# Kernel optimization log

Hardware: AMD Instinct MI355X
Metric: run time of the kernel (lower is better)

The kernel has to match this reference:

```python
import jax, jax.numpy as jnp
import numpy as np

B, S, H = 8, 128, 768  # batch, seq_len, hidden (guide==vis)
EPS = 1e-12


def setup_inputs() -> dict:
    key = jax.random.key(0)
    ks = jax.random.split(key, 5)
    return {
        "seq_hiddens_x": jax.random.normal(ks[0], (B, S, H), jnp.float32),
        "seq_hiddens_y": jax.random.normal(ks[1], (B, S, H), jnp.float32),
        "cat_W": jax.random.normal(ks[2], (H, 2 * H), jnp.float32) * 0.02,
        "cat_b": jnp.zeros((H,), jnp.float32),
        "beta": jnp.zeros((H,), jnp.float32),
        "gamma": jnp.ones((H,), jnp.float32),
        "beta_W": jax.random.normal(ks[3], (H, H), jnp.float32) * 0.02,
        "gamma_W": jax.random.normal(ks[4], (H, H), jnp.float32) * 0.02,
    }


def reference(seq_hiddens_x, seq_hiddens_y, cat_W, cat_b, beta, gamma, beta_W, gamma_W):
    s = seq_hiddens_x.shape[1]
    # upper_reg2seq: flatten upper-triangular (i<=j) pairs, row-major
    ii, jj = np.triu_indices(s)
    guide = seq_hiddens_x[:, ii, :]    # (B, P, H)
    visible = seq_hiddens_y[:, jj, :]  # (B, P, H)

    # 'cat' branch: relu(Linear([guide; visible]))
    cat_pre = jax.nn.relu(
        jnp.einsum('bph,oh->bpo', jnp.concatenate([guide, visible], axis=-1), cat_W) + cat_b
    )

    # 'cln' branch: conditional LayerNorm(visible, cond=guide)
    # NOTE: original code uses std = (var + eps)**2 (not sqrt) -- replicated faithfully.
    b = jnp.einsum('bph,oh->bpo', guide, beta_W) + beta
    g = jnp.einsum('bph,oh->bpo', guide, gamma_W) + gamma
    mean = jnp.mean(visible, axis=-1, keepdims=True)
    cen = visible - mean
    var = jnp.mean(cen * cen, axis=-1, keepdims=True)
    std = (var + EPS) ** 2
    cln_pre = cen / std * g + b

    return (cat_pre + cln_pre) / 2.0
```

## Files before the change

kernel.cpp:

```cpp
#include <hip/hip_runtime.h>
#include <hip/hip_bf16.h>
#include <math.h>
#include <stdint.h>

#define S_LEN 128
#define H_DIM 768
#define B_DIM 8
#define NPAIR 8256
#define MROWS 1024
#define NTOT  3072
#define EPSC  1e-12f

typedef __bf16 bf16x8 __attribute__((ext_vector_type(8)));
typedef float  f32x4  __attribute__((ext_vector_type(4)));

static __device__ __forceinline__ unsigned short f2bf(float f) {
  union { float f; unsigned u; } a; a.f = f;
  unsigned u = a.u;
  u += 0x7fffu + ((u >> 16) & 1u);
  return (unsigned short)(u >> 16);
}

__global__ __launch_bounds__(256) void convert_xy(const float* __restrict__ x,
                                                  const float* __restrict__ y,
                                                  unsigned short* __restrict__ xb,
                                                  unsigned short* __restrict__ yb) {
  int idx = blockIdx.x * 256 + threadIdx.x;
  if (idx >= MROWS * H_DIM / 4) return;
  float4 vx = ((const float4*)x)[idx];
  float4 vy = ((const float4*)y)[idx];
  ushort4 ox; ox.x = f2bf(vx.x); ox.y = f2bf(vx.y); ox.z = f2bf(vx.z); ox.w = f2bf(vx.w);
  ushort4 oy; oy.x = f2bf(vy.x); oy.y = f2bf(vy.y); oy.z = f2bf(vy.z); oy.w = f2bf(vy.w);
  ((ushort4*)xb)[idx] = ox;
  ((ushort4*)yb)[idx] = oy;
}

__global__ __launch_bounds__(256) void pack_w(const float* __restrict__ catW,
                                              const float* __restrict__ betaW,
                                              const float* __restrict__ gammaW,
                                              unsigned short* __restrict__ Wb) {
  int idx = blockIdx.x * 256 + threadIdx.x;
  if (idx >= NTOT * H_DIM / 4) return;
  int e = idx * 4;
  int n = e / H_DIM, k = e % H_DIM;
  const float* src;
  if      (n < 768)  src = catW   + (size_t)n * 1536 + k;
  else if (n < 1536) src = betaW  + (size_t)(n - 768) * 768 + k;
  else if (n < 2304) src = gammaW + (size_t)(n - 1536) * 768 + k;
  else               src = catW   + (size_t)(n - 2304) * 1536 + 768 + k;
  float4 v = *(const float4*)src;
  ushort4 o; o.x = f2bf(v.x); o.y = f2bf(v.y); o.z = f2bf(v.z); o.w = f2bf(v.w);
  *(ushort4*)(Wb + e) = o;
}

__global__ __launch_bounds__(256) void row_stats(const float* __restrict__ y,
                                                 float* __restrict__ mean,
                                                 float* __restrict__ inv) {
  int row = blockIdx.x;
  const float* yr = y + (size_t)row * H_DIM;
  float s = 0.f, s2 = 0.f;
  for (int o = threadIdx.x; o < H_DIM; o += 256) { float v = yr[o]; s += v; s2 += v * v; }
  for (int off = 32; off > 0; off >>= 1) { s += __shfl_down(s, off); s2 += __shfl_down(s2, off); }
  __shared__ float ls[4], ls2[4];
  if ((threadIdx.x & 63) == 0) { ls[threadIdx.x >> 6] = s; ls2[threadIdx.x >> 6] = s2; }
  __syncthreads();
  if (threadIdx.x == 0) {
    float S1 = ls[0] + ls[1] + ls[2] + ls[3];
    float S2 = ls2[0] + ls2[1] + ls2[2] + ls2[3];
    float m = S1 / H_DIM;
    float var = S2 / H_DIM - m * m;
    float st = var + EPSC;
    mean[row] = m;
    inv[row] = 1.0f / (st * st);
  }
}

__device__ __forceinline__ void gload_lds16(const void* g, void* l) {
  __builtin_amdgcn_global_load_lds(
      (const __attribute__((address_space(1))) unsigned int*)(uintptr_t)g,
      (__attribute__((address_space(3))) unsigned int*)(uintptr_t)l,
      16, 0, 0);
}

__global__ __launch_bounds__(256) void gemm_bt(const unsigned short* __restrict__ Xb,
                                               const unsigned short* __restrict__ Yb,
                                               const unsigned short* __restrict__ Wb,
                                               float* __restrict__ P) {
  __shared__ unsigned short As[128 * 32];
  __shared__ unsigned short Bs[128 * 32];
  const int m0 = blockIdx.x * 128;
  const int n0 = blockIdx.y * 128;
  const unsigned short* A = (n0 < 2304) ? Xb : Yb;
  const unsigned short* Arow = A + (size_t)m0 * H_DIM;
  const unsigned short* Brow = Wb + (size_t)n0 * H_DIM;

  const int tid  = threadIdx.x;
  const int lane = tid & 63;
  const int wave = tid >> 6;
  const int wm = (wave >> 1) * 64;
  const int wn = (wave & 1) * 64;
  const int quad = lane >> 4;
  const int r    = lane & 15;

  const int ar = tid >> 2;
  const int ac = (tid & 3) * 8;

  f32x4 acc[4][4] = {};

  for (int k0 = 0; k0 < H_DIM; k0 += 32) {
    gload_lds16(Arow + (size_t)ar * H_DIM + k0 + ac,        &As[tid * 8]);
    gload_lds16(Arow + (size_t)(ar + 64) * H_DIM + k0 + ac, &As[2048 + tid * 8]);
    gload_lds16(Brow + (size_t)ar * H_DIM + k0 + ac,        &Bs[tid * 8]);
    gload_lds16(Brow + (size_t)(ar + 64) * H_DIM + k0 + ac, &Bs[2048 + tid * 8]);
    __syncthreads();

    bf16x8 af[4], bfr[4];
#pragma unroll
    for (int mi = 0; mi < 4; ++mi)
      af[mi] = *(const bf16x8*)&As[(wm + mi * 16 + r) * 32 + quad * 8];
#pragma unroll
    for (int ni = 0; ni < 4; ++ni)
      bfr[ni] = *(const bf16x8*)&Bs[(wn + ni * 16 + r) * 32 + quad * 8];
#pragma unroll
    for (int mi = 0; mi < 4; ++mi)
#pragma unroll
      for (int ni = 0; ni < 4; ++ni)
        acc[mi][ni] = __builtin_amdgcn_mfma_f32_16x16x32_bf16(af[mi], bfr[ni], acc[mi][ni], 0, 0, 0);
    __syncthreads();
  }

#pragma unroll
  for (int mi = 0; mi < 4; ++mi) {
#pragma unroll
    for (int ni = 0; ni < 4; ++ni) {
      const int row = m0 + wm + mi * 16 + quad * 4;
      const int col = n0 + wn + ni * 16 + r;
#pragma unroll
      for (int reg = 0; reg < 4; ++reg)
        P[(size_t)(row + reg) * NTOT + col] = acc[mi][ni][reg];
    }
  }
}

__global__ __launch_bounds__(192) void epilogue(const float* __restrict__ P,
                                                const float* __restrict__ Yf,
                                                const float* __restrict__ mean,
                                                const float* __restrict__ inv,
                                                const float* __restrict__ cat_b,
                                                const float* __restrict__ beta,
                                                const float* __restrict__ gamma,
                                                float* __restrict__ out) {
  const int p = blockIdx.x;
  const int b = blockIdx.y;
  int i = (int)((2.0 * S_LEN + 1.0
                 - sqrt((2.0 * S_LEN + 1.0) * (2.0 * S_LEN + 1.0) - 8.0 * (double)p)) * 0.5);
  if (i < 0) i = 0;
  if (i > S_LEN - 1) i = S_LEN - 1;
  while ((i + 1) * (2 * S_LEN - i) / 2 <= p) ++i;
  while (i * (2 * S_LEN - i + 1) / 2 > p) --i;
  const int j = i + (p - i * (2 * S_LEN - i + 1) / 2);

  const int o = threadIdx.x * 4;
  const size_t ri = (size_t)(b * S_LEN + i) * NTOT;
  const size_t rj = (size_t)(b * S_LEN + j) * NTOT;
  float4 ax = *(const float4*)(P + ri + o);
  float4 bx = *(const float4*)(P + ri + 768 + o);
  float4 gx = *(const float4*)(P + ri + 1536 + o);
  float4 ay = *(const float4*)(P + rj + 2304 + o);
  float4 yv = *(const float4*)(Yf + (size_t)(b * S_LEN + j) * H_DIM + o);
  const float m  = mean[b * S_LEN + j];
  const float iv = inv[b * S_LEN + j];
  float4 cb = *(const float4*)(cat_b + o);
  float4 be = *(const float4*)(beta + o);
  float4 ga = *(const float4*)(gamma + o);
  float4 rr;
  rr.x = 0.5f * (fmaxf(ax.x + ay.x + cb.x, 0.f) + (yv.x - m) * iv * (gx.x + ga.x) + bx.x + be.x);
  rr.y = 0.5f * (fmaxf(ax.y + ay.y + cb.y, 0.f) + (yv.y - m) * iv * (gx.y + ga.y) + bx.y + be.y);
  rr.z = 0.5f * (fmaxf(ax.z + ay.z + cb.z, 0.f) + (yv.z - m) * iv * (gx.z + ga.z) + bx.z + be.z);
  rr.w = 0.5f * (fmaxf(ax.w + ay.w + cb.w, 0.f) + (yv.w - m) * iv * (gx.w + ga.w) + bx.w + be.w);
  *(float4*)(out + ((size_t)b * NPAIR + p) * H_DIM + o) = rr;
}

extern "C" void kernel_launch(void* const* d_in, const int* in_sizes, int n_in,
                              void* d_out, int out_size, void* d_ws, size_t ws_size,
                              hipStream_t stream) {
  const float* x      = (const float*)d_in[0];
  const float* y      = (const float*)d_in[1];
  const float* catW   = (const float*)d_in[2];
  const float* catb   = (const float*)d_in[3];
  const float* beta   = (const float*)d_in[4];
  const float* gamma  = (const float*)d_in[5];
  const float* betaW  = (const float*)d_in[6];
  const float* gammaW = (const float*)d_in[7];

  char* ws = (char*)d_ws;
  unsigned short* Xb   = (unsigned short*)(ws);
  unsigned short* Yb   = (unsigned short*)(ws + 1572864);
  unsigned short* Wb   = (unsigned short*)(ws + 3145728);
  float*          P    = (float*)(ws + 7864320);
  float*          mean = (float*)(ws + 20447232);
  float*          inv  = (float*)(ws + 20451328);
  float*          out  = (float*)d_out;

  convert_xy<<<768, 256, 0, stream>>>(x, y, Xb, Yb);
  pack_w<<<2304, 256, 0, stream>>>(catW, betaW, gammaW, Wb);
  row_stats<<<1024, 256, 0, stream>>>(y, mean, inv);
  gemm_bt<<<dim3(8, 24), 256, 0, stream>>>(Xb, Yb, Wb, P);
  epilogue<<<dim3(NPAIR, B_DIM), 192, 0, stream>>>(P, y, mean, inv, catb, beta, gamma, out);
}
```

Measured before the change: 277.9 us.

## Fuse prep kernels, shrink GEMM tiles, store bf16 intermediates, chunk epilogue pairs

Merges the x/y conversion, weight packing and row statistics into one prep launch. Shrinks GEMM tiles to 64x64 so the grid has more blocks. Stores the projection buffer P in bf16 instead of fp32 to halve its traffic. The epilogue now handles 8 pairs per block, reusing the guide-row loads and amortising the index math. Rounding the projections to bf16 adds precision loss before the relu and the layer-norm combination.

```diff
diff --git a/kernel.cpp b/kernel.cpp
--- a/kernel.cpp
+++ b/kernel.cpp
@@ -10,6 +10,7 @@
 #define MROWS 1024
 #define NTOT  3072
 #define EPSC  1e-12f
+#define CHUNK 8
 
 typedef __bf16 bf16x8 __attribute__((ext_vector_type(8)));
 typedef float  f32x4  __attribute__((ext_vector_type(4)));
@@ -20,58 +21,67 @@
   u += 0x7fffu + ((u >> 16) & 1u);
   return (unsigned short)(u >> 16);
 }
-
-__global__ __launch_bounds__(256) void convert_xy(const float* __restrict__ x,
-                                                  const float* __restrict__ y,
-                                                  unsigned short* __restrict__ xb,
-                                                  unsigned short* __restrict__ yb) {
-  int idx = blockIdx.x * 256 + threadIdx.x;
-  if (idx >= MROWS * H_DIM / 4) return;
-  float4 vx = ((const float4*)x)[idx];
-  float4 vy = ((const float4*)y)[idx];
-  ushort4 ox; ox.x = f2bf(vx.x); ox.y = f2bf(vx.y); ox.z = f2bf(vx.z); ox.w = f2bf(vx.w);
-  ushort4 oy; oy.x = f2bf(vy.x); oy.y = f2bf(vy.y); oy.z = f2bf(vy.z); oy.w = f2bf(vy.w);
-  ((ushort4*)xb)[idx] = ox;
-  ((ushort4*)yb)[idx] = oy;
-}
-
-__global__ __launch_bounds__(256) void pack_w(const float* __restrict__ catW,
-                                              const float* __restrict__ betaW,
-                                              const float* __restrict__ gammaW,
-                                              unsigned short* __restrict__ Wb) {
-  int idx = blockIdx.x * 256 + threadIdx.x;
-  if (idx >= NTOT * H_DIM / 4) return;
-  int e = idx * 4;
-  int n = e / H_DIM, k = e % H_DIM;
-  const float* src;
-  if      (n < 768)  src = catW   + (size_t)n * 1536 + k;
-  else if (n < 1536) src = betaW  + (size_t)(n - 768) * 768 + k;
-  else if (n < 2304) src = gammaW + (size_t)(n - 1536) * 768 + k;
-  else               src = catW   + (size_t)(n - 2304) * 1536 + 768 + k;
-  float4 v = *(const float4*)src;
-  ushort4 o; o.x = f2bf(v.x); o.y = f2bf(v.y); o.z = f2bf(v.z); o.w = f2bf(v.w);
-  *(ushort4*)(Wb + e) = o;
-}
-
-__global__ __launch_bounds__(256) void row_stats(const float* __restrict__ y,
-                                                 float* __restrict__ mean,
-                                                 float* __restrict__ inv) {
-  int row = blockIdx.x;
-  const float* yr = y + (size_t)row * H_DIM;
-  float s = 0.f, s2 = 0.f;
-  for (int o = threadIdx.x; o < H_DIM; o += 256) { float v = yr[o]; s += v; s2 += v * v; }
-  for (int off = 32; off > 0; off >>= 1) { s += __shfl_down(s, off); s2 += __shfl_down(s2, off); }
-  __shared__ float ls[4], ls2[4];
-  if ((threadIdx.x & 63) == 0) { ls[threadIdx.x >> 6] = s; ls2[threadIdx.x >> 6] = s2; }
-  __syncthreads();
-  if (threadIdx.x == 0) {
-    float S1 = ls[0] + ls[1] + ls[2] + ls[3];
-    float S2 = ls2[0] + ls2[1] + ls2[2] + ls2[3];
-    float m = S1 / H_DIM;
-    float var = S2 / H_DIM - m * m;
-    float st = var + EPSC;
-    mean[row] = m;
-    inv[row] = 1.0f / (st * st);
+static __device__ __forceinline__ float bf2f(unsigned short s) {
+  union { unsigned u; float f; } a; a.u = ((unsigned)s) << 16;
+  return a.f;
+}
+static __device__ __forceinline__ float4 ld_bf4(const unsigned short* p) {
+  ushort4 u = *(const ushort4*)p;
+  float4 f; f.x = bf2f(u.x); f.y = bf2f(u.y); f.z = bf2f(u.z); f.w = bf2f(u.w);
+  return f;
+}
+
+__global__ __launch_bounds__(256) void prep(const float* __restrict__ x,
+                                            const float* __restrict__ y,
+                                            const float* __restrict__ catW,
+                                            const float* __restrict__ betaW,
+                                            const float* __restrict__ gammaW,
+                                            unsigned short* __restrict__ Xb,
+                                            unsigned short* __restrict__ Yb,
+                                            unsigned short* __restrict__ Wb,
+                                            float* __restrict__ mean,
+                                            float* __restrict__ inv) {
+  const int bid = blockIdx.x;
+  const int tid = threadIdx.x;
+  if (bid < MROWS) {
+    const int row = bid;
+    float s = 0.f, s2 = 0.f;
+    if (tid < 192) {
+      const int o = tid * 4;
+      float4 vx = *(const float4*)(x + (size_t)row * H_DIM + o);
+      float4 vy = *(const float4*)(y + (size_t)row * H_DIM + o);
+      ushort4 ox; ox.x = f2bf(vx.x); ox.y = f2bf(vx.y); ox.z = f2bf(vx.z); ox.w = f2bf(vx.w);
+      ushort4 oy; oy.x = f2bf(vy.x); oy.y = f2bf(vy.y); oy.z = f2bf(vy.z); oy.w = f2bf(vy.w);
+      *(ushort4*)(Xb + (size_t)row * H_DIM + o) = ox;
+      *(ushort4*)(Yb + (size_t)row * H_DIM + o) = oy;
+      s  = vy.x + vy.y + vy.z + vy.w;
+      s2 = vy.x * vy.x + vy.y * vy.y + vy.z * vy.z + vy.w * vy.w;
+    }
+    for (int off = 32; off > 0; off >>= 1) { s += __shfl_down(s, off); s2 += __shfl_down(s2, off); }
+    __shared__ float ls[4], ls2[4];
+    if ((tid & 63) == 0) { ls[tid >> 6] = s; ls2[tid >> 6] = s2; }
+    __syncthreads();
+    if (tid == 0) {
+      float S1 = ls[0] + ls[1] + ls[2] + ls[3];
+      float S2 = ls2[0] + ls2[1] + ls2[2] + ls2[3];
+      float m = S1 / H_DIM;
+      float var = S2 / H_DIM - m * m;
+      float st = var + EPSC;
+      mean[row] = m;
+      inv[row] = 1.0f / (st * st);
+    }
+  } else {
+    int idx = (bid - MROWS) * 256 + tid;
+    int e = idx * 4;
+    int n = e / H_DIM, k = e % H_DIM;
+    const float* src;
+    if      (n < 768)  src = catW   + (size_t)n * 1536 + k;
+    else if (n < 1536) src = betaW  + (size_t)(n - 768) * 768 + k;
+    else if (n < 2304) src = gammaW + (size_t)(n - 1536) * 768 + k;
+    else               src = catW   + (size_t)(n - 2304) * 1536 + 768 + k;
+    float4 v = *(const float4*)src;
+    ushort4 o; o.x = f2bf(v.x); o.y = f2bf(v.y); o.z = f2bf(v.z); o.w = f2bf(v.w);
+    *(ushort4*)(Wb + e) = o;
   }
 }
 
@@ -85,11 +95,11 @@
 __global__ __launch_bounds__(256) void gemm_bt(const unsigned short* __restrict__ Xb,
                                                const unsigned short* __restrict__ Yb,
                                                const unsigned short* __restrict__ Wb,
-                                               float* __restrict__ P) {
-  __shared__ unsigned short As[128 * 32];
-  __shared__ unsigned short Bs[128 * 32];
-  const int m0 = blockIdx.x * 128;
-  const int n0 = blockIdx.y * 128;
+                                               unsigned short* __restrict__ P) {
+  __shared__ unsigned short As[64 * 32];
+  __shared__ unsigned short Bs[64 * 32];
+  const int m0 = blockIdx.x * 64;
+  const int n0 = blockIdx.y * 64;
   const unsigned short* A = (n0 < 2304) ? Xb : Yb;
   const unsigned short* Arow = A + (size_t)m0 * H_DIM;
   const unsigned short* Brow = Wb + (size_t)n0 * H_DIM;
@@ -97,52 +107,50 @@
   const int tid  = threadIdx.x;
   const int lane = tid & 63;
   const int wave = tid >> 6;
-  const int wm = (wave >> 1) * 64;
-  const int wn = (wave & 1) * 64;
+  const int wm = (wave >> 1) * 32;
+  const int wn = (wave & 1) * 32;
   const int quad = lane >> 4;
   const int r    = lane & 15;
 
   const int ar = tid >> 2;
   const int ac = (tid & 3) * 8;
 
-  f32x4 acc[4][4] = {};
+  f32x4 acc[2][2] = {};
 
   for (int k0 = 0; k0 < H_DIM; k0 += 32) {
-    gload_lds16(Arow + (size_t)ar * H_DIM + k0 + ac,        &As[tid * 8]);
-    gload_lds16(Arow + (size_t)(ar + 64) * H_DIM + k0 + ac, &As[2048 + tid * 8]);
-    gload_lds16(Brow + (size_t)ar * H_DIM + k0 + ac,        &Bs[tid * 8]);
-    gload_lds16(Brow + (size_t)(ar + 64) * H_DIM + k0 + ac, &Bs[2048 + tid * 8]);
+    gload_lds16(Arow + (size_t)ar * H_DIM + k0 + ac, &As[tid * 8]);
+    gload_lds16(Brow + (size_t)ar * H_DIM + k0 + ac, &Bs[tid * 8]);
     __syncthreads();
 
-    bf16x8 af[4], bfr[4];
-#pragma unroll
-    for (int mi = 0; mi < 4; ++mi)
+    bf16x8 af[2], bfr[2];
+#pragma unroll
+    for (int mi = 0; mi < 2; ++mi)
       af[mi] = *(const bf16x8*)&As[(wm + mi * 16 + r) * 32 + quad * 8];
 #pragma unroll
-    for (int ni = 0; ni < 4; ++ni)
+    for (int ni = 0; ni < 2; ++ni)
       bfr[ni] = *(const bf16x8*)&Bs[(wn + ni * 16 + r) * 32 + quad * 8];
 #pragma unroll
-    for (int mi = 0; mi < 4; ++mi)
-#pragma unroll
-      for (int ni = 0; ni < 4; ++ni)
+    for (int mi = 0; mi < 2; ++mi)
+#pragma unroll
+      for (int ni = 0; ni < 2; ++ni)
         acc[mi][ni] = __builtin_amdgcn_mfma_f32_16x16x32_bf16(af[mi], bfr[ni], acc[mi][ni], 0, 0, 0);
     __syncthreads();
   }
 
 #pragma unroll
-  for (int mi = 0; mi < 4; ++mi) {
-#pragma unroll
-    for (int ni = 0; ni < 4; ++ni) {
+  for (int mi = 0; mi < 2; ++mi) {
+#pragma unroll
+    for (int ni = 0; ni < 2; ++ni) {
       const int row = m0 + wm + mi * 16 + quad * 4;
       const int col = n0 + wn + ni * 16 + r;
 #pragma unroll
       for (int reg = 0; reg < 4; ++reg)
-        P[(size_t)(row + reg) * NTOT + col] = acc[mi][ni][reg];
-    }
-  }
-}
-
-__global__ __launch_bounds__(192) void epilogue(const float* __restrict__ P,
+        P[(size_t)(row + reg) * NTOT + col] = f2bf(acc[mi][ni][reg]);
+    }
+  }
+}
+
+__global__ __launch_bounds__(192) void epilogue(const unsigned short* __restrict__ P,
                                                 const float* __restrict__ Yf,
                                                 const float* __restrict__ mean,
                                                 const float* __restrict__ inv,
@@ -150,35 +158,49 @@
                                                 const float* __restrict__ beta,
                                                 const float* __restrict__ gamma,
                                                 float* __restrict__ out) {
-  const int p = blockIdx.x;
-  const int b = blockIdx.y;
-  int i = (int)((2.0 * S_LEN + 1.0
-                 - sqrt((2.0 * S_LEN + 1.0) * (2.0 * S_LEN + 1.0) - 8.0 * (double)p)) * 0.5);
+  const int b  = blockIdx.y;
+  const int p0 = blockIdx.x * CHUNK;
+  const int o  = threadIdx.x * 4;
+
+  int i = (int)((257.0 - sqrt(257.0 * 257.0 - 8.0 * (double)p0)) * 0.5);
   if (i < 0) i = 0;
   if (i > S_LEN - 1) i = S_LEN - 1;
-  while ((i + 1) * (2 * S_LEN - i) / 2 <= p) ++i;
-  while (i * (2 * S_LEN - i + 1) / 2 > p) --i;
-  const int j = i + (p - i * (2 * S_LEN - i + 1) / 2);
-
-  const int o = threadIdx.x * 4;
-  const size_t ri = (size_t)(b * S_LEN + i) * NTOT;
-  const size_t rj = (size_t)(b * S_LEN + j) * NTOT;
-  float4 ax = *(const float4*)(P + ri + o);
-  float4 bx = *(const float4*)(P + ri + 768 + o);
-  float4 gx = *(const float4*)(P + ri + 1536 + o);
-  float4 ay = *(const float4*)(P + rj + 2304 + o);
-  float4 yv = *(const float4*)(Yf + (size_t)(b * S_LEN + j) * H_DIM + o);
-  const float m  = mean[b * S_LEN + j];
-  const float iv = inv[b * S_LEN + j];
+  while ((i + 1) * (256 - i) / 2 <= p0) ++i;
+  while (i * (257 - i) / 2 > p0) --i;
+
   float4 cb = *(const float4*)(cat_b + o);
   float4 be = *(const float4*)(beta + o);
   float4 ga = *(const float4*)(gamma + o);
-  float4 rr;
-  rr.x = 0.5f * (fmaxf(ax.x + ay.x + cb.x, 0.f) + (yv.x - m) * iv * (gx.x + ga.x) + bx.x + be.x);
-  rr.y = 0.5f * (fmaxf(ax.y + ay.y + cb.y, 0.f) + (yv.y - m) * iv * (gx.y + ga.y) + bx.y + be.y);
-  rr.z = 0.5f * (fmaxf(ax.z + ay.z + cb.z, 0.f) + (yv.z - m) * iv * (gx.z + ga.z) + bx.z + be.z);
-  rr.w = 0.5f * (fmaxf(ax.w + ay.w + cb.w, 0.f) + (yv.w - m) * iv * (gx.w + ga.w) + bx.w + be.w);
-  *(float4*)(out + ((size_t)b * NPAIR + p) * H_DIM + o) = rr;
+
+  size_t ri = (size_t)(b * S_LEN + i) * NTOT;
+  float4 ax = ld_bf4(P + ri + o);
+  float4 bx = ld_bf4(P + ri + 768 + o);
+  float4 gx = ld_bf4(P + ri + 1536 + o);
+
+#pragma unroll
+  for (int t = 0; t < CHUNK; ++t) {
+    const int p = p0 + t;
+    bool moved = false;
+    while ((i + 1) * (256 - i) / 2 <= p) { ++i; moved = true; }
+    if (moved) {
+      ri = (size_t)(b * S_LEN + i) * NTOT;
+      ax = ld_bf4(P + ri + o);
+      bx = ld_bf4(P + ri + 768 + o);
+      gx = ld_bf4(P + ri + 1536 + o);
+    }
+    const int j = i + (p - i * (257 - i) / 2);
+    const int rowj = b * S_LEN + j;
+    float4 ay = ld_bf4(P + (size_t)rowj * NTOT + 2304 + o);
+    float4 yv = *(const float4*)(Yf + (size_t)rowj * H_DIM + o);
+    const float m  = mean[rowj];
+    const float iv = inv[rowj];
+    float4 rr;
+    rr.x = 0.5f * (fmaxf(ax.x + ay.x + cb.x, 0.f) + (yv.x - m) * iv * (gx.x + ga.x) + bx.x + be.x);
+    rr.y = 0.5f * (fmaxf(ax.y + ay.y + cb.y, 0.f) + (yv.y - m) * iv * (gx.y + ga.y) + bx.y + be.y);
+    rr.z = 0.5f * (fmaxf(ax.z + ay.z + cb.z, 0.f) + (yv.z - m) * iv * (gx.z + ga.z) + bx.z + be.z);
+    rr.w = 0.5f * (fmaxf(ax.w + ay.w + cb.w, 0.f) + (yv.w - m) * iv * (gx.w + ga.w) + bx.w + be.w);
+    *(float4*)(out + ((size_t)b * NPAIR + p) * H_DIM + o) = rr;
+  }
 }
 
 extern "C" void kernel_launch(void* const* d_in, const int* in_sizes, int n_in,
@@ -197,14 +219,12 @@
   unsigned short* Xb   = (unsigned short*)(ws);
   unsigned short* Yb   = (unsigned short*)(ws + 1572864);
   unsigned short* Wb   = (unsigned short*)(ws + 3145728);
-  float*          P    = (float*)(ws + 7864320);
-  float*          mean = (float*)(ws + 20447232);
-  float*          inv  = (float*)(ws + 20451328);
+  unsigned short* P    = (unsigned short*)(ws + 7864320);
+  float*          mean = (float*)(ws + 14155776);
+  float*          inv  = (float*)(ws + 14159872);
   float*          out  = (float*)d_out;
 
-  convert_xy<<<768, 256, 0, stream>>>(x, y, Xb, Yb);
-  pack_w<<<2304, 256, 0, stream>>>(catW, betaW, gammaW, Wb);
-  row_stats<<<1024, 256, 0, stream>>>(y, mean, inv);
-  gemm_bt<<<dim3(8, 24), 256, 0, stream>>>(Xb, Yb, Wb, P);
-  epilogue<<<dim3(NPAIR, B_DIM), 192, 0, stream>>>(P, y, mean, inv, catb, beta, gamma, out);
-}
+  prep<<<MROWS + 2304, 256, 0, stream>>>(x, y, catW, betaW, gammaW, Xb, Yb, Wb, mean, inv);
+  gemm_bt<<<dim3(16, 48), 256, 0, stream>>>(Xb, Yb, Wb, P);
+  epilogue<<<dim3(NPAIR / CHUNK, B_DIM), 192, 0, stream>>>(P, y, mean, inv, catb, beta, gamma, out);
+}
```

After: 239.2 us. -13.9%, faster.
